# Kernel optimization log

Measured on AMD Instinct MI355X. Metric: run time of the kernel, lower is better.

## Reference

```python
import jax, jax.numpy as jnp
import numpy as np

K0, K1 = 3, 3  # kernel_size
UNITS = K0 * K1


def setup_inputs() -> dict:
    key = jax.random.key(0)
    k1, k2, k3 = jax.random.split(key, 3)
    B, S = 100, 512  # batch fixed to 100 by the original code's np.zeros((100,1)) pad
    inputs = jax.random.normal(k1, (B, S, S, 1), dtype=jnp.float32)
    # per-position unshared weights/bias, 'random_normal' initializer (stddev 0.05)
    w = jax.random.normal(k2, (S * S * UNITS,), dtype=jnp.float32) * 0.05
    b = jax.random.normal(k3, (S * S * UNITS,), dtype=jnp.float32) * 0.05
    return {"inputs": inputs, "w": w, "b": b}


def reference(inputs, w, b):
    # Faithful to the original (including its quirks):
    #  - taps read diagonal entries inputs[:, j+t, j+t] for t in [0, UNITS)
    #    (tmp_j is never reset across the m loop)
    #  - validity mask uses (tmp_i = i + t//K1, tmp_j = j + t)
    #  - bias b is added BEFORE reduce_sum over units, so
    #    out[b,i,j] = UNITS * dot(v, w_ij) + sum(b_ij)
    B, W, H, C = inputs.shape  # C == 1, W == H
    t = jnp.arange(UNITS)
    diag = inputs[:, jnp.arange(H), jnp.arange(H), 0]          # (B, H)
    jj = jnp.arange(H)[:, None] + t[None, :]                   # (H, UNITS) tmp_j
    valid_j = jj < H
    gathered = jnp.where(valid_j[None], diag[:, jnp.minimum(jj, H - 1)], 0.0)  # (B,H,UNITS)
    ii = jnp.arange(W)[:, None] + (t // K1)[None, :]           # (W, UNITS) tmp_i
    valid_i = (ii < W).astype(inputs.dtype)
    w3 = w.reshape(W, H, UNITS) * valid_i[:, None, :]          # mask taps by tmp_i bound
    dot = jnp.einsum('bjt,ijt->bij', gathered, w3)             # (B, W, H)
    bias = b.reshape(W, H, UNITS).sum(-1)                      # (W, H)
    out = UNITS * dot + bias[None]
    return out.reshape(B, W * H)  # position order: i * tmp_h + j
```

## Files before the change

### kernel.cpp

```cpp
#include <hip/hip_runtime.h>

#define S 512
#define SP 520
#define UNITS 9
#define BLOCK 256
#define BCHUNK 10

__global__ void diag_extract_kernel(const float* __restrict__ in,
                                    float* __restrict__ diag, int B) {
    int idx = blockIdx.x * blockDim.x + threadIdx.x;
    if (idx < B * SP) {
        int b = idx / SP;
        int j = idx - b * SP;
        diag[idx] = (j < S) ? in[(size_t)b * S * S + (size_t)j * (S + 1)] : 0.f;
    }
}

template<bool USE_WS>
__global__ __launch_bounds__(BLOCK) void cnn_main_kernel(
        const float* __restrict__ w, const float* __restrict__ bv,
        const float* __restrict__ diag, const float* __restrict__ raw_in,
        float* __restrict__ out, int B) {
    __shared__ __align__(16) float sdiag[USE_WS ? 1 : SP];

    const int group = blockIdx.x & ((S / 4) - 1);
    const int chunk = blockIdx.x >> 7;
    const int row   = threadIdx.x >> 6;
    const int lane  = threadIdx.x & 63;
    const int i     = group * 4 + row;
    const int jA    = 4 * lane;
    const int jB    = 256 + 4 * lane;

    float wv[72];
    {
        const float4* wa = reinterpret_cast<const float4*>(w + (size_t)(i * S + jA) * UNITS);
        const float4* wb = reinterpret_cast<const float4*>(w + (size_t)(i * S + jB) * UNITS);
        #pragma unroll
        for (int q = 0; q < 9; ++q) {
            float4 va = wa[q], vb = wb[q];
            wv[4*q+0] = va.x; wv[4*q+1] = va.y; wv[4*q+2] = va.z; wv[4*q+3] = va.w;
            wv[36+4*q+0] = vb.x; wv[36+4*q+1] = vb.y; wv[36+4*q+2] = vb.z; wv[36+4*q+3] = vb.w;
        }
    }
    if (i >= S - 2) {
        const int tmax = (i == S - 1) ? 3 : 6;
        #pragma unroll
        for (int h = 0; h < 2; ++h)
            #pragma unroll
            for (int r = 0; r < 4; ++r)
                #pragma unroll
                for (int t = 0; t < UNITS; ++t)
                    if (t >= tmax) wv[36*h + r*UNITS + t] = 0.f;
    }

    float bias[8];
    {
        float tmp[72];
        const float4* ba = reinterpret_cast<const float4*>(bv + (size_t)(i * S + jA) * UNITS);
        const float4* bb = reinterpret_cast<const float4*>(bv + (size_t)(i * S + jB) * UNITS);
        #pragma unroll
        for (int q = 0; q < 9; ++q) {
            float4 va = ba[q], vb = bb[q];
            tmp[4*q+0] = va.x; tmp[4*q+1] = va.y; tmp[4*q+2] = va.z; tmp[4*q+3] = va.w;
            tmp[36+4*q+0] = vb.x; tmp[36+4*q+1] = vb.y; tmp[36+4*q+2] = vb.z; tmp[36+4*q+3] = vb.w;
        }
        #pragma unroll
        for (int r = 0; r < 8; ++r) {
            float s = 0.f;
            #pragma unroll
            for (int t = 0; t < UNITS; ++t) s += tmp[r * UNITS + t];
            bias[r] = s;
        }
    }

    const int b0 = chunk * BCHUNK;
    for (int bb = 0; bb < BCHUNK; ++bb) {
        const int b = b0 + bb;
        if (b >= B) break;

        const float* p;
        if (USE_WS) {
            p = diag + (size_t)b * SP;
        } else {
            __syncthreads();
            for (int idx = threadIdx.x; idx < SP; idx += BLOCK)
                sdiag[idx] = (idx < S) ? raw_in[(size_t)b * S * S + (size_t)idx * (S + 1)] : 0.f;
            __syncthreads();
            p = sdiag;
        }

        float dA[12], dB[12];
        {
            const float4* pa = reinterpret_cast<const float4*>(p + jA);
            const float4* pb = reinterpret_cast<const float4*>(p + jB);
            #pragma unroll
            for (int q = 0; q < 3; ++q) {
                float4 va = pa[q], vb = pb[q];
                dA[4*q+0] = va.x; dA[4*q+1] = va.y; dA[4*q+2] = va.z; dA[4*q+3] = va.w;
                dB[4*q+0] = vb.x; dB[4*q+1] = vb.y; dB[4*q+2] = vb.z; dB[4*q+3] = vb.w;
            }
        }

        float4 resA, resB;
        float* rA = &resA.x; float* rB = &resB.x;
        #pragma unroll
        for (int r = 0; r < 4; ++r) {
            float accA = 0.f, accB = 0.f;
            #pragma unroll
            for (int t = 0; t < UNITS; ++t) {
                accA = fmaf(dA[r + t], wv[r * UNITS + t], accA);
                accB = fmaf(dB[r + t], wv[36 + r * UNITS + t], accB);
            }
            rA[r] = fmaf(accA, (float)UNITS, bias[r]);
            rB[r] = fmaf(accB, (float)UNITS, bias[4 + r]);
        }

        float* orow = out + (size_t)b * S * S + (size_t)i * S;
        *reinterpret_cast<float4*>(orow + jA) = resA;
        *reinterpret_cast<float4*>(orow + jB) = resB;
    }
}

extern "C" void kernel_launch(void* const* d_in, const int* in_sizes, int n_in,
                              void* d_out, int out_size, void* d_ws, size_t ws_size,
                              hipStream_t stream) {
    const float* in = (const float*)d_in[0];
    const float* w  = (const float*)d_in[1];
    const float* bv = (const float*)d_in[2];
    float* out      = (float*)d_out;

    const int B = in_sizes[0] / (S * S);
    const int nchunk = (B + BCHUNK - 1) / BCHUNK;
    dim3 grid((S / 4) * nchunk);

    if (ws_size >= (size_t)B * SP * sizeof(float)) {
        float* diag = (float*)d_ws;
        diag_extract_kernel<<<(B * SP + 255) / 256, 256, 0, stream>>>(in, diag, B);
        cnn_main_kernel<true><<<grid, BLOCK, 0, stream>>>(w, bv, diag, in, out, B);
    } else {
        cnn_main_kernel<false><<<grid, BLOCK, 0, stream>>>(w, bv, nullptr, in, out, B);
    }
}
```

Measured before the change: 207.3 us.

## Transpose weights and presum bias in a fused prep kernel before main pass

Adds a prep kernel that extracts the diagonal, transposes the per-position weights into a tap-major layout with the row mask applied, and presums the bias into a workspace. The main kernel then loads weights with coalesced float4 reads and no bias reduction, and each thread handles 4 outputs instead of 8, which cuts register pressure and may raise occupancy. The cost is an extra full pass over the weights and biases (about 20 MB of traffic) on every call, plus a larger workspace requirement.

New measurement: 198.8 us. 4.1% less time.

```diff
diff --git a/kernel.cpp b/kernel.cpp
--- a/kernel.cpp
+++ b/kernel.cpp
@@ -3,121 +3,177 @@
 #define S 512
 #define SP 520
 #define UNITS 9
-#define BLOCK 256
 #define BCHUNK 10
 
-__global__ void diag_extract_kernel(const float* __restrict__ in,
-                                    float* __restrict__ diag, int B) {
-    int idx = blockIdx.x * blockDim.x + threadIdx.x;
-    if (idx < B * SP) {
-        int b = idx / SP;
-        int j = idx - b * SP;
-        diag[idx] = (j < S) ? in[(size_t)b * S * S + (size_t)j * (S + 1)] : 0.f;
-    }
-}
-
-template<bool USE_WS>
-__global__ __launch_bounds__(BLOCK) void cnn_main_kernel(
+#define WT_OFF   (0x40000)
+#define BIAS_OFF (WT_OFF + UNITS * S * S * 4)
+#define WS_NEED  (BIAS_OFF + S * S * 4)
+
+__global__ __launch_bounds__(256) void prep_kernel(
         const float* __restrict__ w, const float* __restrict__ bv,
-        const float* __restrict__ diag, const float* __restrict__ raw_in,
-        float* __restrict__ out, int B) {
-    __shared__ __align__(16) float sdiag[USE_WS ? 1 : SP];
-
-    const int group = blockIdx.x & ((S / 4) - 1);
-    const int chunk = blockIdx.x >> 7;
-    const int row   = threadIdx.x >> 6;
-    const int lane  = threadIdx.x & 63;
-    const int i     = group * 4 + row;
-    const int jA    = 4 * lane;
-    const int jB    = 256 + 4 * lane;
-
-    float wv[72];
-    {
-        const float4* wa = reinterpret_cast<const float4*>(w + (size_t)(i * S + jA) * UNITS);
-        const float4* wb = reinterpret_cast<const float4*>(w + (size_t)(i * S + jB) * UNITS);
-        #pragma unroll
-        for (int q = 0; q < 9; ++q) {
-            float4 va = wa[q], vb = wb[q];
-            wv[4*q+0] = va.x; wv[4*q+1] = va.y; wv[4*q+2] = va.z; wv[4*q+3] = va.w;
-            wv[36+4*q+0] = vb.x; wv[36+4*q+1] = vb.y; wv[36+4*q+2] = vb.z; wv[36+4*q+3] = vb.w;
-        }
-    }
-    if (i >= S - 2) {
-        const int tmax = (i == S - 1) ? 3 : 6;
-        #pragma unroll
-        for (int h = 0; h < 2; ++h)
-            #pragma unroll
-            for (int r = 0; r < 4; ++r)
-                #pragma unroll
-                for (int t = 0; t < UNITS; ++t)
-                    if (t >= tmax) wv[36*h + r*UNITS + t] = 0.f;
-    }
-
-    float bias[8];
-    {
-        float tmp[72];
-        const float4* ba = reinterpret_cast<const float4*>(bv + (size_t)(i * S + jA) * UNITS);
-        const float4* bb = reinterpret_cast<const float4*>(bv + (size_t)(i * S + jB) * UNITS);
-        #pragma unroll
-        for (int q = 0; q < 9; ++q) {
-            float4 va = ba[q], vb = bb[q];
-            tmp[4*q+0] = va.x; tmp[4*q+1] = va.y; tmp[4*q+2] = va.z; tmp[4*q+3] = va.w;
-            tmp[36+4*q+0] = vb.x; tmp[36+4*q+1] = vb.y; tmp[36+4*q+2] = vb.z; tmp[36+4*q+3] = vb.w;
-        }
-        #pragma unroll
-        for (int r = 0; r < 8; ++r) {
-            float s = 0.f;
-            #pragma unroll
-            for (int t = 0; t < UNITS; ++t) s += tmp[r * UNITS + t];
-            bias[r] = s;
-        }
-    }
+        const float* __restrict__ in, float* __restrict__ diag,
+        float* __restrict__ w_t, float* __restrict__ bias_sum, int B) {
+    __shared__ __align__(16) float sw[S * UNITS];
+    __shared__ __align__(16) float sb[S * UNITS];
+
+    const int i   = blockIdx.x;
+    const int tid = threadIdx.x;
+
+    {
+        int idx = blockIdx.x * 256 + tid;
+        if (idx < B * SP) {
+            int b = idx / SP;
+            int j = idx - b * SP;
+            diag[idx] = (j < S) ? in[(size_t)b * S * S + (size_t)j * (S + 1)] : 0.f;
+        }
+    }
+
+    {
+        const float4* wr = reinterpret_cast<const float4*>(w + (size_t)i * S * UNITS);
+        const float4* br = reinterpret_cast<const float4*>(bv + (size_t)i * S * UNITS);
+        float4* sw4 = reinterpret_cast<float4*>(sw);
+        float4* sb4 = reinterpret_cast<float4*>(sb);
+        for (int q = tid; q < S * UNITS / 4; q += 256) {
+            sw4[q] = wr[q];
+            sb4[q] = br[q];
+        }
+    }
+    __syncthreads();
+
+    const int tmax = min(UNITS, 3 * (S - i));
+    for (int j = tid; j < S; j += 256) {
+        float s = 0.f;
+        #pragma unroll
+        for (int t = 0; t < UNITS; ++t) s += sb[j * UNITS + t];
+        bias_sum[(size_t)i * S + j] = s;
+        #pragma unroll
+        for (int t = 0; t < UNITS; ++t) {
+            float v = (t < tmax) ? sw[j * UNITS + t] : 0.f;
+            w_t[(size_t)t * S * S + (size_t)i * S + j] = v;
+        }
+    }
+}
+
+__global__ __launch_bounds__(256) void cnn_main_kernel(
+        const float* __restrict__ w_t, const float* __restrict__ bias_sum,
+        const float* __restrict__ diag, float* __restrict__ out, int B) {
+    const int group = blockIdx.x & ((S / 2) - 1);
+    const int chunk = blockIdx.x >> 8;
+    const int r     = threadIdx.x >> 7;
+    const int jl    = threadIdx.x & 127;
+    const int i     = group * 2 + r;
+    const int j0    = jl * 4;
+
+    float4 wt[UNITS];
+    #pragma unroll
+    for (int t = 0; t < UNITS; ++t)
+        wt[t] = *reinterpret_cast<const float4*>(
+            w_t + (size_t)t * S * S + (size_t)i * S + j0);
+    const float4 bias = *reinterpret_cast<const float4*>(
+        bias_sum + (size_t)i * S + j0);
+
+    const float* wv = reinterpret_cast<const float*>(wt);
 
     const int b0 = chunk * BCHUNK;
     for (int bb = 0; bb < BCHUNK; ++bb) {
         const int b = b0 + bb;
         if (b >= B) break;
 
-        const float* p;
-        if (USE_WS) {
-            p = diag + (size_t)b * SP;
-        } else {
-            __syncthreads();
-            for (int idx = threadIdx.x; idx < SP; idx += BLOCK)
-                sdiag[idx] = (idx < S) ? raw_in[(size_t)b * S * S + (size_t)idx * (S + 1)] : 0.f;
-            __syncthreads();
-            p = sdiag;
-        }
-
-        float dA[12], dB[12];
+        float dv[12];
         {
-            const float4* pa = reinterpret_cast<const float4*>(p + jA);
-            const float4* pb = reinterpret_cast<const float4*>(p + jB);
+            const float4* p = reinterpret_cast<const float4*>(diag + (size_t)b * SP + j0);
             #pragma unroll
             for (int q = 0; q < 3; ++q) {
-                float4 va = pa[q], vb = pb[q];
-                dA[4*q+0] = va.x; dA[4*q+1] = va.y; dA[4*q+2] = va.z; dA[4*q+3] = va.w;
-                dB[4*q+0] = vb.x; dB[4*q+1] = vb.y; dB[4*q+2] = vb.z; dB[4*q+3] = vb.w;
+                float4 v = p[q];
+                dv[4*q+0] = v.x; dv[4*q+1] = v.y; dv[4*q+2] = v.z; dv[4*q+3] = v.w;
             }
         }
 
-        float4 resA, resB;
-        float* rA = &resA.x; float* rB = &resB.x;
-        #pragma unroll
-        for (int r = 0; r < 4; ++r) {
-            float accA = 0.f, accB = 0.f;
-            #pragma unroll
-            for (int t = 0; t < UNITS; ++t) {
-                accA = fmaf(dA[r + t], wv[r * UNITS + t], accA);
-                accB = fmaf(dB[r + t], wv[36 + r * UNITS + t], accB);
-            }
-            rA[r] = fmaf(accA, (float)UNITS, bias[r]);
-            rB[r] = fmaf(accB, (float)UNITS, bias[4 + r]);
-        }
-
-        float* orow = out + (size_t)b * S * S + (size_t)i * S;
-        *reinterpret_cast<float4*>(orow + jA) = resA;
-        *reinterpret_cast<float4*>(orow + jB) = resB;
+        float4 res;
+        float* rp = &res.x;
+        const float* bp = &bias.x;
+        #pragma unroll
+        for (int k = 0; k < 4; ++k) {
+            float acc = 0.f;
+            #pragma unroll
+            for (int t = 0; t < UNITS; ++t)
+                acc = fmaf(dv[k + t], wv[t * 4 + k], acc);
+            rp[k] = fmaf(acc, (float)UNITS, bp[k]);
+        }
+
+        *reinterpret_cast<float4*>(out + (size_t)b * S * S + (size_t)i * S + j0) = res;
+    }
+}
+
+__global__ __launch_bounds__(256) void cnn_fallback_kernel(
+        const float* __restrict__ w, const float* __restrict__ bv,
+        const float* __restrict__ raw_in, float* __restrict__ out, int B) {
+    __shared__ __align__(16) float sdiag[SP];
+    const int group = blockIdx.x & ((S / 2) - 1);
+    const int chunk = blockIdx.x >> 8;
+    const int r     = threadIdx.x >> 7;
+    const int jl    = threadIdx.x & 127;
+    const int i     = group * 2 + r;
+    const int j0    = jl * 4;
+
+    float wv[4 * UNITS];
+    {
+        const float4* ws4 = reinterpret_cast<const float4*>(w + (size_t)(i * S + j0) * UNITS);
+        #pragma unroll
+        for (int q = 0; q < 9; ++q) {
+            float4 v = ws4[q];
+            wv[4*q] = v.x; wv[4*q+1] = v.y; wv[4*q+2] = v.z; wv[4*q+3] = v.w;
+        }
+    }
+    if (i >= S - 2) {
+        const int tmax = 3 * (S - i);
+        #pragma unroll
+        for (int k = 0; k < 4; ++k)
+            #pragma unroll
+            for (int t = 0; t < UNITS; ++t)
+                if (t >= tmax) wv[k * UNITS + t] = 0.f;
+    }
+    float bias[4];
+    {
+        float tmp[4 * UNITS];
+        const float4* bs4 = reinterpret_cast<const float4*>(bv + (size_t)(i * S + j0) * UNITS);
+        #pragma unroll
+        for (int q = 0; q < 9; ++q) {
+            float4 v = bs4[q];
+            tmp[4*q] = v.x; tmp[4*q+1] = v.y; tmp[4*q+2] = v.z; tmp[4*q+3] = v.w;
+        }
+        #pragma unroll
+        for (int k = 0; k < 4; ++k) {
+            float s = 0.f;
+            #pragma unroll
+            for (int t = 0; t < UNITS; ++t) s += tmp[k * UNITS + t];
+            bias[k] = s;
+        }
+    }
+    const int b0 = chunk * BCHUNK;
+    for (int bb = 0; bb < BCHUNK; ++bb) {
+        const int b = b0 + bb;
+        if (b >= B) break;
+        __syncthreads();
+        for (int idx = threadIdx.x; idx < SP; idx += 256)
+            sdiag[idx] = (idx < S) ? raw_in[(size_t)b * S * S + (size_t)idx * (S + 1)] : 0.f;
+        __syncthreads();
+        float dv[12];
+        #pragma unroll
+        for (int q = 0; q < 3; ++q) {
+            float4 v = reinterpret_cast<const float4*>(&sdiag[j0])[q];
+            dv[4*q] = v.x; dv[4*q+1] = v.y; dv[4*q+2] = v.z; dv[4*q+3] = v.w;
+        }
+        float4 res; float* rp = &res.x;
+        #pragma unroll
+        for (int k = 0; k < 4; ++k) {
+            float acc = 0.f;
+            #pragma unroll
+            for (int t = 0; t < UNITS; ++t)
+                acc = fmaf(dv[k + t], wv[k * UNITS + t], acc);
+            rp[k] = fmaf(acc, (float)UNITS, bias[k]);
+        }
+        *reinterpret_cast<float4*>(out + (size_t)b * S * S + (size_t)i * S + j0) = res;
     }
 }
 
@@ -131,13 +187,16 @@
 
     const int B = in_sizes[0] / (S * S);
     const int nchunk = (B + BCHUNK - 1) / BCHUNK;
-    dim3 grid((S / 4) * nchunk);
-
-    if (ws_size >= (size_t)B * SP * sizeof(float)) {
-        float* diag = (float*)d_ws;
-        diag_extract_kernel<<<(B * SP + 255) / 256, 256, 0, stream>>>(in, diag, B);
-        cnn_main_kernel<true><<<grid, BLOCK, 0, stream>>>(w, bv, diag, in, out, B);
+    dim3 grid((S / 2) * nchunk);
+
+    if (ws_size >= (size_t)WS_NEED) {
+        char* ws = (char*)d_ws;
+        float* diag     = (float*)(ws);
+        float* w_t      = (float*)(ws + WT_OFF);
+        float* bias_sum = (float*)(ws + BIAS_OFF);
+        prep_kernel<<<S, 256, 0, stream>>>(w, bv, in, diag, w_t, bias_sum, B);
+        cnn_main_kernel<<<grid, 256, 0, stream>>>(w_t, bias_sum, diag, out, B);
     } else {
-        cnn_main_kernel<false><<<grid, BLOCK, 0, stream>>>(w, bv, nullptr, in, out, B);
-    }
-}
+        cnn_fallback_kernel<<<grid, 256, 0, stream>>>(w, bv, in, out, B);
+    }
+}
```
